# Performance work log

Hardware: AMD Instinct MI355X
Metric: run time of the kernel (lower is better)

Reference implementation:

```python
import jax, jax.numpy as jnp
import numpy as np

B, S, V, E, H = 1024, 256, 32000, 300, 256  # batch, enc_len, vocab, embed_dim, hidden_dim
ENC = 3 * H  # encoder feature width (768)


def setup_inputs() -> dict:
    key = jax.random.key(0)
    ks = jax.random.split(key, 14)
    s = 0.02
    return {
        "x": jax.random.randint(ks[0], (B,), 0, V),
        "h": jax.random.normal(ks[1], (B, H), jnp.float32),
        "c": jax.random.normal(ks[2], (B, H), jnp.float32),
        "encoder_outputs": jax.random.normal(ks[3], (B, S, ENC), jnp.float32),
        "emb": jax.random.normal(ks[4], (V, E), jnp.float32) * s,
        "attn_w": jax.random.normal(ks[5], (H, 4 * H), jnp.float32) * s,
        "attn_b": jnp.zeros((H,), jnp.float32),
        "v_w": jax.random.normal(ks[6], (H,), jnp.float32) * s,
        "w_ih": jax.random.normal(ks[7], (4 * H, E + ENC), jnp.float32) * s,
        "w_hh": jax.random.normal(ks[8], (4 * H, H), jnp.float32) * s,
        "b_ih": jnp.zeros((4 * H,), jnp.float32),
        "b_hh": jnp.zeros((4 * H,), jnp.float32),
        "out_w": jax.random.normal(ks[9], (V, H), jnp.float32) * s,
        "out_b": jnp.zeros((V,), jnp.float32),
    }


def reference(x, h, c, encoder_outputs, emb, attn_w, attn_b, v_w,
              w_ih, w_hh, b_ih, b_hh, out_w, out_b):
    # embedding (dropout is identity in eval mode)
    e = emb[x]  # [B, E]
    # additive attention: tanh(W [h; enc] + b); split W to avoid materializing the concat
    w_h, w_e = attn_w[:, :H], attn_w[:, H:]
    energy = jnp.tanh(h @ w_h.T[:, :] [None].squeeze(0) @ jnp.eye(H, dtype=h.dtype) if False else
                      (h @ w_h.T)[:, None, :] + jnp.einsum('bsd,hd->bsh', encoder_outputs, w_e) + attn_b)  # [B,S,H]
    scores = jnp.einsum('bsh,h->bs', energy, v_w)
    attn = jax.nn.softmax(scores, axis=1)  # [B,S]
    context = jnp.einsum('bs,bsd->bd', attn, encoder_outputs)  # [B, 3H]
    # single-step LSTM (PyTorch gate order: i, f, g, o)
    xi = jnp.concatenate([e, context], axis=-1)  # [B, E+3H]
    gates = xi @ w_ih.T + b_ih + h @ w_hh.T + b_hh  # [B, 4H]
    i, f, g, o = jnp.split(gates, 4, axis=-1)
    c2 = jax.nn.sigmoid(f) * c + jax.nn.sigmoid(i) * jnp.tanh(g)
    h2 = jax.nn.sigmoid(o) * jnp.tanh(c2)
    logits = h2 @ out_w.T + out_b  # [B, V]
    return logits, h2, c2
```

## Files before the change

### kernel.cpp

```cpp
#include <hip/hip_runtime.h>
#include <hip/hip_bf16.h>
#include <stdint.h>

#define BDIM 1024
#define SDIM 256
#define VDIM 32000
#define EDIM 300
#define HDIM 256
#define ENCD 768
#define G4H  1024
#define KXI  1344

typedef short bf16x8 __attribute__((ext_vector_type(8)));
typedef float f32x4  __attribute__((ext_vector_type(4)));

static __device__ __forceinline__ unsigned short f2bf(float f) {
  __hip_bfloat16 b = __float2bfloat16(f);
  return *reinterpret_cast<unsigned short*>(&b);
}
static __device__ __forceinline__ unsigned pk2(float x, float y) {
  float2 f; f.x = x; f.y = y;
  __hip_bfloat162 h = __float22bfloat162_rn(f);
  return *reinterpret_cast<unsigned*>(&h);
}
static __device__ __forceinline__ float bf2f(unsigned short u) {
  union { unsigned u; float f; } v; v.u = ((unsigned)u) << 16; return v.f;
}
static __device__ __forceinline__ float sigf(float x) {
  return 1.0f / (1.0f + __expf(-x));
}
static __device__ __forceinline__ float tanh_fast(float x) {
  return 1.0f - 2.0f / (__expf(2.0f * x) + 1.0f);
}
static __device__ __forceinline__ int swz_off(int row, int kbyte) {
  return row * 1536 + (kbyte ^ ((row & 7) << 4));
}

__global__ void k_prep(const float* __restrict__ attn_w, const float* __restrict__ w_ih,
                       const float* __restrict__ w_hh, const float* __restrict__ out_w,
                       const float* __restrict__ h,
                       unsigned short* __restrict__ w_e_frag, unsigned short* __restrict__ w_h_b,
                       unsigned short* __restrict__ h_b,
                       unsigned short* __restrict__ Wb, unsigned short* __restrict__ outw_b) {
  const long NWE = (long)HDIM * ENCD;
  const long NW1 = (long)HDIM * HDIM;
  const long NHB = (long)BDIM * HDIM;
  const long NWB = (long)G4H * KXI;
  const long NOW = (long)VDIM * HDIM;
  const long total = NWE + NW1 + NHB + NWB + NOW;
  for (long idx = blockIdx.x * 256L + threadIdx.x; idx < total; idx += gridDim.x * 256L) {
    long i = idx;
    if (i < NWE) {
      int e    = (int)(i & 7);
      int f    = (int)(i >> 3);
      int lane = f & 63;
      int n    = (f >> 6) & 1;
      int r2   = f >> 7;
      int kt   = r2 % 24;
      int w    = r2 / 24;
      int j    = 32 * w + 16 * n + (lane & 15);
      int k    = 32 * kt + (lane >> 4) * 8 + e;
      w_e_frag[i] = f2bf(attn_w[j * (4 * HDIM) + HDIM + k]);
    } else if ((i -= NWE) < NW1) {
      int j = (int)(i / HDIM), k = (int)(i % HDIM);
      w_h_b[i] = f2bf(attn_w[j * (4 * HDIM) + k]);
    } else if ((i -= NW1) < NHB) {
      h_b[i] = f2bf(h[i]);
    } else if ((i -= NHB) < NWB) {
      int g = (int)(i / KXI), k = (int)(i % KXI);
      float v = 0.f;
      if (k < EDIM + ENCD) v = w_ih[(long)g * (EDIM + ENCD) + k];
      else if (k < EDIM + ENCD + HDIM) v = w_hh[(long)g * HDIM + (k - (EDIM + ENCD))];
      Wb[i] = f2bf(v);
    } else {
      i -= NWB;
      outw_b[i] = f2bf(out_w[i]);
    }
  }
}

__launch_bounds__(512, 4)
__global__ void k_energy_ctx(const float* __restrict__ enc, const unsigned short* __restrict__ w_e_frag,
                             const float* __restrict__ hwb, const float* __restrict__ v_w,
                             float* __restrict__ ctx_part, float* __restrict__ denom_part) {
  const int b = blockIdx.x >> 3;
  const int st = blockIdx.x & 7;
  const int s0 = st * 32;
  const int t = threadIdx.x;
  const int lane = t & 63;
  const int w = t >> 6;
  const int li = lane & 15;
  const int lg = lane >> 4;

  __shared__ __align__(16) unsigned short encT[32 * ENCD];
  __shared__ float scores_lds[8 * 32];
  __shared__ float p_lds[32];

  const float* encB = enc + (long)(b * SDIM + s0) * ENCD;
  const int jw = 32 * w;
  const unsigned short* fragW = w_e_frag + (((long)w * 24 * 2) * 64 + lane) * 8;

  float4 sv[12];
#pragma unroll
  for (int u = 0; u < 12; ++u)
    sv[u] = *(const float4*)(encB + 4 * t + 2048 * u);

  bf16x8 bfr[6][2];
#pragma unroll
  for (int p = 0; p < 6; ++p)
#pragma unroll
    for (int n = 0; n < 2; ++n)
      bfr[p][n] = *(const bf16x8*)(fragW + ((p * 2 + n) * 64) * 8);

  float hw0 = hwb[b * HDIM + jw + li];
  float hw1 = hwb[b * HDIM + jw + 16 + li];
  float vw0 = v_w[jw + li];
  float vw1 = v_w[jw + 16 + li];

#pragma unroll
  for (int u = 0; u < 12; ++u) {
    const int flat = 4 * t + 2048 * u;
    const int row = flat / ENCD;
    const int col = flat - row * ENCD;
    uint2 pk;
    pk.x = pk2(sv[u].x, sv[u].y);
    pk.y = pk2(sv[u].z, sv[u].w);
    *(uint2*)((char*)encT + swz_off(row, col * 2)) = pk;
  }

  f32x4 acc[2][2];
#pragma unroll
  for (int m = 0; m < 2; m++)
#pragma unroll
    for (int n = 0; n < 2; n++) { f32x4 z = {0.f, 0.f, 0.f, 0.f}; acc[m][n] = z; }

  __syncthreads();

  bf16x8 afr[2][2];
#pragma unroll
  for (int p = 0; p < 2; ++p)
#pragma unroll
    for (int m = 0; m < 2; ++m)
      afr[p][m] = *(const bf16x8*)((const char*)encT + swz_off(16 * m + li, (p * 32 + lg * 8) * 2));

#pragma unroll
  for (int kt = 0; kt < 24; ++kt) {
    const int kb = kt % 6, ka = kt & 1;
#pragma unroll
    for (int m = 0; m < 2; m++)
#pragma unroll
      for (int n = 0; n < 2; n++)
        acc[m][n] = __builtin_amdgcn_mfma_f32_16x16x32_bf16(afr[ka][m], bfr[kb][n], acc[m][n], 0, 0, 0);
    if (kt + 6 < 24) {
#pragma unroll
      for (int n = 0; n < 2; ++n)
        bfr[kb][n] = *(const bf16x8*)(fragW + (((kt + 6) * 2 + n) * 64) * 8);
    }
    if (kt + 2 < 24) {
      const int kn2 = (kt + 2) * 32;
#pragma unroll
      for (int m = 0; m < 2; ++m)
        afr[ka][m] = *(const bf16x8*)((const char*)encT + swz_off(16 * m + li, (kn2 + lg * 8) * 2));
    }
  }

  float val[2][4];
#pragma unroll
  for (int m = 0; m < 2; m++)
#pragma unroll
    for (int r = 0; r < 4; r++) {
      float v0 = tanh_fast(acc[m][0][r] + hw0) * vw0 + tanh_fast(acc[m][1][r] + hw1) * vw1;
      v0 += __shfl_xor(v0, 1);
      v0 += __shfl_xor(v0, 2);
      v0 += __shfl_xor(v0, 4);
      v0 += __shfl_xor(v0, 8);
      val[m][r] = v0;
    }
  if (li < 4) {
    scores_lds[w * 32 + 4 * lg + li]      = val[0][li];
    scores_lds[w * 32 + 16 + 4 * lg + li] = val[1][li];
  }
  __syncthreads();
  if (t < 32) {
    float sc = 0.f;
#pragma unroll
    for (int ww = 0; ww < 8; ++ww) sc += scores_lds[ww * 32 + t];
    float p = __expf(sc);
    p_lds[t] = p;
    float dsum = p;
    dsum += __shfl_xor(dsum, 1);
    dsum += __shfl_xor(dsum, 2);
    dsum += __shfl_xor(dsum, 4);
    dsum += __shfl_xor(dsum, 8);
    dsum += __shfl_xor(dsum, 16);
    if (t == 0) denom_part[b * 8 + st] = dsum;
  }
  __syncthreads();
  if (t < 384) {
    float cx = 0.f, cy = 0.f;
#pragma unroll
    for (int s = 0; s < 32; ++s) {
      float p = p_lds[s];
      unsigned u = *(const unsigned*)((const char*)encT + swz_off(s, 4 * t));
      cx += p * bf2f((unsigned short)(u & 0xffffu));
      cy += p * bf2f((unsigned short)(u >> 16));
    }
    float* cp = ctx_part + (long)(b * 8 + st) * ENCD + 2 * t;
    cp[0] = cx; cp[1] = cy;
  }
}

__global__ void k_xi(const int* __restrict__ x, const float* __restrict__ emb,
                     const float* __restrict__ h, const float* __restrict__ ctx_part,
                     const float* __restrict__ denom_part, unsigned short* __restrict__ xi_b) {
  int b = blockIdx.x, t = threadIdx.x;
  float denom = 0.f;
#pragma unroll
  for (int st = 0; st < 8; ++st) denom += denom_part[b * 8 + st];
  float inv = 1.0f / denom;
#pragma unroll
  for (int u = 0; u < 3; ++u) {
    int d = t + 256 * u;
    float s = 0.f;
#pragma unroll
    for (int st = 0; st < 8; ++st) s += ctx_part[(long)(b * 8 + st) * ENCD + d];
    xi_b[(long)b * KXI + EDIM + d] = f2bf(s * inv);
  }
  int xv = x[b];
  for (int cc = t; cc < EDIM; cc += 256)
    xi_b[(long)b * KXI + cc] = f2bf(emb[(long)xv * EDIM + cc]);
  xi_b[(long)b * KXI + EDIM + ENCD + t] = f2bf(h[b * HDIM + t]);
  if (t < KXI - (EDIM + ENCD + HDIM))
    xi_b[(long)b * KXI + (EDIM + ENCD + HDIM) + t] = 0;
}

__launch_bounds__(256)
__global__ void k_gemm_bt(const unsigned short* __restrict__ A, const unsigned short* __restrict__ Bt,
                          const float* __restrict__ bias1, const float* __restrict__ bias2,
                          float* __restrict__ out, int N, int K, int MTILES) {
  int bx = blockIdx.x;
  int mt = bx % MTILES, nt = bx / MTILES;
  int row0 = mt * 128, col0 = nt * 128;
  int t = threadIdx.x, lane = t & 63, w = t >> 6;
  int li = lane & 15, lg = lane >> 4;
  int wr = (w >> 1) * 64, wc = (w & 1) * 64;
  __shared__ __align__(16) unsigned short As[2][128 * 32];
  __shared__ __align__(16) unsigned short Bs[2][128 * 32];
  f32x4 acc[4][4];
#pragma unroll
  for (int m = 0; m < 4; m++)
#pragma unroll
    for (int n = 0; n < 4; n++) { f32x4 z = {0.f, 0.f, 0.f, 0.f}; acc[m][n] = z; }

  auto stage = [&](int buf, int k0) {
#pragma unroll
    for (int rep = 0; rep < 2; ++rep) {
      int slot = t + rep * 256;
      int r = slot >> 2, sg = slot & 3;
      uint4 va = *(const uint4*)(A + (long)(row0 + r) * K + k0 + sg * 8);
      uint4 vb = *(const uint4*)(Bt + (long)(col0 + r) * K + k0 + sg * 8);
      *(uint4*)&As[buf][r * 32 + sg * 8] = va;
      *(uint4*)&Bs[buf][r * 32 + sg * 8] = vb;
    }
  };

  stage(0, 0);
  __syncthreads();
  const int nk = K / 32;
  for (int kt = 0; kt < nk; ++kt) {
    if (kt + 1 < nk) stage((kt + 1) & 1, (kt + 1) * 32);
    int cb = kt & 1;
    bf16x8 a[4], bb[4];
#pragma unroll
    for (int m = 0; m < 4; m++) a[m] = *(const bf16x8*)&As[cb][(wr + 16 * m + li) * 32 + lg * 8];
#pragma unroll
    for (int n = 0; n < 4; n++) bb[n] = *(const bf16x8*)&Bs[cb][(wc + 16 * n + li) * 32 + lg * 8];
#pragma unroll
    for (int m = 0; m < 4; m++)
#pragma unroll
      for (int n = 0; n < 4; n++)
        acc[m][n] = __builtin_amdgcn_mfma_f32_16x16x32_bf16(a[m], bb[n], acc[m][n], 0, 0, 0);
    __syncthreads();
  }

#pragma unroll
  for (int n = 0; n < 4; n++) {
    int col = col0 + wc + 16 * n + li;
    float bs = bias1[col];
    if (bias2) bs += bias2[col];
#pragma unroll
    for (int m = 0; m < 4; m++) {
      int rb = row0 + wr + 16 * m + lg * 4;
#pragma unroll
      for (int r = 0; r < 4; r++)
        out[(long)(rb + r) * N + col] = acc[m][n][r] + bs;
    }
  }
}

__global__ void k_lstm(const float* __restrict__ gates, const float* __restrict__ c,
                       float* __restrict__ h2, float* __restrict__ c2,
                       unsigned short* __restrict__ h2b) {
  int b = blockIdx.x, j = threadIdx.x;
  const float* g = gates + (long)b * G4H;
  float ig = sigf(g[j]);
  float fg = sigf(g[HDIM + j]);
  float gg = tanh_fast(g[2 * HDIM + j]);
  float og = sigf(g[3 * HDIM + j]);
  float cv = c[b * HDIM + j];
  float c2v = fg * cv + ig * gg;
  float h2v = og * tanh_fast(c2v);
  c2[b * HDIM + j] = c2v;
  h2[b * HDIM + j] = h2v;
  h2b[b * HDIM + j] = f2bf(h2v);
}

extern "C" void kernel_launch(void* const* d_in, const int* in_sizes, int n_in,
                              void* d_out, int out_size, void* d_ws, size_t ws_size,
                              hipStream_t stream) {
  const int*   x      = (const int*)d_in[0];
  const float* h      = (const float*)d_in[1];
  const float* c      = (const float*)d_in[2];
  const float* enc    = (const float*)d_in[3];
  const float* emb    = (const float*)d_in[4];
  const float* attn_w = (const float*)d_in[5];
  const float* attn_b = (const float*)d_in[6];
  const float* v_w    = (const float*)d_in[7];
  const float* w_ih   = (const float*)d_in[8];
  const float* w_hh   = (const float*)d_in[9];
  const float* b_ih   = (const float*)d_in[10];
  const float* b_hh   = (const float*)d_in[11];
  const float* out_w  = (const float*)d_in[12];
  const float* out_b  = (const float*)d_in[13];
  float* out = (float*)d_out;

  char* ws = (char*)d_ws;
  float* hwb             = (float*)(ws + 0);
  unsigned short* w_e_fr = (unsigned short*)(ws + 1048576);
  unsigned short* w_h_b  = (unsigned short*)(ws + 1441792);
  unsigned short* h_b    = (unsigned short*)(ws + 1572864);
  float* ctx_part        = (float*)(ws + 2097152);
  float* denom_part      = (float*)(ws + 27262976);
  unsigned short* Wb     = (unsigned short*)(ws + 27295744);
  unsigned short* xi_b   = (unsigned short*)(ws + 30048256);
  float* gates           = (float*)(ws + 32800768);
  unsigned short* h2b    = (unsigned short*)(ws + 36995072);
  unsigned short* outw_b = (unsigned short*)(ws + 37519360);
  if (ws_size < 53903360u) return;

  k_prep<<<2048, 256, 0, stream>>>(attn_w, w_ih, w_hh, out_w, h, w_e_fr, w_h_b, h_b, Wb, outw_b);
  k_gemm_bt<<<16, 256, 0, stream>>>(h_b, w_h_b, attn_b, nullptr, hwb, HDIM, HDIM, 8);
  k_energy_ctx<<<8192, 512, 0, stream>>>(enc, w_e_fr, hwb, v_w, ctx_part, denom_part);
  k_xi<<<1024, 256, 0, stream>>>(x, emb, h, ctx_part, denom_part, xi_b);
  k_gemm_bt<<<64, 256, 0, stream>>>(xi_b, Wb, b_ih, b_hh, gates, G4H, KXI, 8);
  k_lstm<<<1024, 256, 0, stream>>>(gates, c, out + (long)BDIM * VDIM,
                                   out + (long)BDIM * VDIM + (long)BDIM * HDIM, h2b);
  k_gemm_bt<<<2000, 256, 0, stream>>>(h2b, outw_b, out_b, nullptr, out, VDIM, HDIM, 8);
}
```

Measured before the change: 382.2 us.

## Make attention kernel persistent with async global-to-LDS prefetch and fused context reduction

Replaces the 8192-block energy/context kernel with 256 persistent blocks, each handling 32 consecutive (batch, seq-tile) units. The next encoder tile is prefetched straight into LDS with global_load_lds, so the load overlaps the current tile's MFMA work. Context and softmax denominator are accumulated in LDS across the 8 seq tiles of each batch row and written to xi_b as normalized bf16. This removes the ctx_part/denom_part round trip and the k_xi kernel, whose embedding, h and padding copies move into k_prep. In exchange occupancy drops to one 512-thread block per CU, with a large LDS footprint, and the loop becomes serial within each block.

Result: slower. 426.4 us (+11.5%).

```diff
diff --git a/kernel.cpp b/kernel.cpp
--- a/kernel.cpp
+++ b/kernel.cpp
@@ -14,6 +14,9 @@
 typedef short bf16x8 __attribute__((ext_vector_type(8)));
 typedef float f32x4  __attribute__((ext_vector_type(4)));
 
+typedef __attribute__((address_space(3))) void       lds_void;
+typedef const __attribute__((address_space(1))) void gbl_void;
+
 static __device__ __forceinline__ unsigned short f2bf(float f) {
   __hip_bfloat16 b = __float2bfloat16(f);
   return *reinterpret_cast<unsigned short*>(&b);
@@ -35,19 +38,30 @@
 static __device__ __forceinline__ int swz_off(int row, int kbyte) {
   return row * 1536 + (kbyte ^ ((row & 7) << 4));
 }
+static __device__ __forceinline__ void lds_barrier() {
+  asm volatile("s_waitcnt lgkmcnt(0)" ::: "memory");
+  __builtin_amdgcn_sched_barrier(0);
+  __builtin_amdgcn_s_barrier();
+  __builtin_amdgcn_sched_barrier(0);
+}
 
 __global__ void k_prep(const float* __restrict__ attn_w, const float* __restrict__ w_ih,
                        const float* __restrict__ w_hh, const float* __restrict__ out_w,
-                       const float* __restrict__ h,
+                       const float* __restrict__ h, const int* __restrict__ x,
+                       const float* __restrict__ emb,
                        unsigned short* __restrict__ w_e_frag, unsigned short* __restrict__ w_h_b,
                        unsigned short* __restrict__ h_b,
-                       unsigned short* __restrict__ Wb, unsigned short* __restrict__ outw_b) {
+                       unsigned short* __restrict__ Wb, unsigned short* __restrict__ outw_b,
+                       unsigned short* __restrict__ xi_b) {
   const long NWE = (long)HDIM * ENCD;
   const long NW1 = (long)HDIM * HDIM;
   const long NHB = (long)BDIM * HDIM;
   const long NWB = (long)G4H * KXI;
   const long NOW = (long)VDIM * HDIM;
-  const long total = NWE + NW1 + NHB + NWB + NOW;
+  const long NEM = (long)BDIM * EDIM;
+  const long NH2 = (long)BDIM * HDIM;
+  const long NPD = (long)BDIM * (KXI - (EDIM + ENCD + HDIM));
+  const long total = NWE + NW1 + NHB + NWB + NOW + NEM + NH2 + NPD;
   for (long idx = blockIdx.x * 256L + threadIdx.x; idx < total; idx += gridDim.x * 256L) {
     long i = idx;
     if (i < NWE) {
@@ -72,166 +86,187 @@
       if (k < EDIM + ENCD) v = w_ih[(long)g * (EDIM + ENCD) + k];
       else if (k < EDIM + ENCD + HDIM) v = w_hh[(long)g * HDIM + (k - (EDIM + ENCD))];
       Wb[i] = f2bf(v);
+    } else if ((i -= NWB) < NOW) {
+      outw_b[i] = f2bf(out_w[i]);
+    } else if ((i -= NOW) < NEM) {
+      int b = (int)(i / EDIM), cc = (int)(i % EDIM);
+      xi_b[(long)b * KXI + cc] = f2bf(emb[(long)x[b] * EDIM + cc]);
+    } else if ((i -= NEM) < NH2) {
+      int b = (int)(i / HDIM), j = (int)(i % HDIM);
+      xi_b[(long)b * KXI + EDIM + ENCD + j] = f2bf(h[(long)b * HDIM + j]);
     } else {
-      i -= NWB;
-      outw_b[i] = f2bf(out_w[i]);
-    }
-  }
-}
-
-__launch_bounds__(512, 4)
+      i -= NH2;
+      const int PADW = KXI - (EDIM + ENCD + HDIM);
+      int b = (int)(i / PADW), p = (int)(i % PADW);
+      xi_b[(long)b * KXI + EDIM + ENCD + HDIM + p] = 0;
+    }
+  }
+}
+
+__launch_bounds__(512, 1)
 __global__ void k_energy_ctx(const float* __restrict__ enc, const unsigned short* __restrict__ w_e_frag,
                              const float* __restrict__ hwb, const float* __restrict__ v_w,
-                             float* __restrict__ ctx_part, float* __restrict__ denom_part) {
-  const int b = blockIdx.x >> 3;
-  const int st = blockIdx.x & 7;
-  const int s0 = st * 32;
+                             unsigned short* __restrict__ xi_b) {
   const int t = threadIdx.x;
   const int lane = t & 63;
   const int w = t >> 6;
   const int li = lane & 15;
   const int lg = lane >> 4;
-
+  const int jw = 32 * w;
+
+  __shared__ __align__(16) float stageF[32 * ENCD];
   __shared__ __align__(16) unsigned short encT[32 * ENCD];
   __shared__ float scores_lds[8 * 32];
   __shared__ float p_lds[32];
-
-  const float* encB = enc + (long)(b * SDIM + s0) * ENCD;
-  const int jw = 32 * w;
-  const unsigned short* fragW = w_e_frag + (((long)w * 24 * 2) * 64 + lane) * 8;
-
-  float4 sv[12];
-#pragma unroll
-  for (int u = 0; u < 12; ++u)
-    sv[u] = *(const float4*)(encB + 4 * t + 2048 * u);
-
-  bf16x8 bfr[6][2];
-#pragma unroll
-  for (int p = 0; p < 6; ++p)
-#pragma unroll
-    for (int n = 0; n < 2; ++n)
-      bfr[p][n] = *(const bf16x8*)(fragW + ((p * 2 + n) * 64) * 8);
-
-  float hw0 = hwb[b * HDIM + jw + li];
-  float hw1 = hwb[b * HDIM + jw + 16 + li];
-  float vw0 = v_w[jw + li];
-  float vw1 = v_w[jw + 16 + li];
-
-#pragma unroll
-  for (int u = 0; u < 12; ++u) {
-    const int flat = 4 * t + 2048 * u;
-    const int row = flat / ENCD;
-    const int col = flat - row * ENCD;
-    uint2 pk;
-    pk.x = pk2(sv[u].x, sv[u].y);
-    pk.y = pk2(sv[u].z, sv[u].w);
-    *(uint2*)((char*)encT + swz_off(row, col * 2)) = pk;
-  }
-
-  f32x4 acc[2][2];
-#pragma unroll
-  for (int m = 0; m < 2; m++)
-#pragma unroll
-    for (int n = 0; n < 2; n++) { f32x4 z = {0.f, 0.f, 0.f, 0.f}; acc[m][n] = z; }
-
-  __syncthreads();
-
-  bf16x8 afr[2][2];
-#pragma unroll
-  for (int p = 0; p < 2; ++p)
-#pragma unroll
-    for (int m = 0; m < 2; ++m)
-      afr[p][m] = *(const bf16x8*)((const char*)encT + swz_off(16 * m + li, (p * 32 + lg * 8) * 2));
-
-#pragma unroll
-  for (int kt = 0; kt < 24; ++kt) {
-    const int kb = kt % 6, ka = kt & 1;
+  __shared__ float ctxAcc[ENCD];
+  __shared__ float hwb_lds[4 * HDIM];
+  __shared__ float denAcc;
+
+  const int NT = 32;
+  const int tile0 = blockIdx.x * NT;
+  const int b0 = tile0 >> 3;
+
+  {
+    const float* src = enc + (long)tile0 * 32 * ENCD;
+#pragma unroll
+    for (int u = 0; u < 12; ++u) {
+      const float* s = src + (u * 512 + t) * 4;
+      char* d = (char*)stageF + (u * 512 + (w << 6)) * 16;
+      __builtin_amdgcn_global_load_lds((gbl_void*)s, (lds_void*)d, 16, 0, 0);
+    }
+  }
+  hwb_lds[t]       = hwb[b0 * HDIM + t];
+  hwb_lds[t + 512] = hwb[b0 * HDIM + t + 512];
+  const float vw0 = v_w[jw + li];
+  const float vw1 = v_w[jw + 16 + li];
+  const unsigned short* fragW = w_e_frag + ((long)w * 3072 + lane) * 8;
+
+  for (int it = 0; it < NT; ++it) {
+    const int tile = tile0 + it;
+    const int b = tile >> 3, st = tile & 7;
+    const bool more = (it + 1 < NT);
+
+    __syncthreads();
+
+    if (st == 0) {
+      if (t < 384) { ctxAcc[2 * t] = 0.f; ctxAcc[2 * t + 1] = 0.f; }
+      if (t == 0) denAcc = 0.f;
+    }
+
+#pragma unroll
+    for (int u = 0; u < 12; ++u) {
+      const int s = u * 512 + t;
+      float4 v = *(const float4*)&stageF[4 * s];
+      const int flat = 4 * s;
+      const int row = flat / ENCD;
+      const int col = flat - row * ENCD;
+      uint2 pk;
+      pk.x = pk2(v.x, v.y);
+      pk.y = pk2(v.z, v.w);
+      *(uint2*)((char*)encT + swz_off(row, col * 2)) = pk;
+    }
+    lds_barrier();
+
+    if (more) {
+      const float* src = enc + (long)(tile + 1) * 32 * ENCD;
+#pragma unroll
+      for (int u = 0; u < 12; ++u) {
+        const float* s = src + (u * 512 + t) * 4;
+        char* d = (char*)stageF + (u * 512 + (w << 6)) * 16;
+        __builtin_amdgcn_global_load_lds((gbl_void*)s, (lds_void*)d, 16, 0, 0);
+      }
+    }
+
+    const float hw0 = hwb_lds[(b - b0) * HDIM + jw + li];
+    const float hw1 = hwb_lds[(b - b0) * HDIM + jw + 16 + li];
+
+    f32x4 acc[2][2];
 #pragma unroll
     for (int m = 0; m < 2; m++)
 #pragma unroll
-      for (int n = 0; n < 2; n++)
-        acc[m][n] = __builtin_amdgcn_mfma_f32_16x16x32_bf16(afr[ka][m], bfr[kb][n], acc[m][n], 0, 0, 0);
-    if (kt + 6 < 24) {
+      for (int n = 0; n < 2; n++) { f32x4 z = {0.f, 0.f, 0.f, 0.f}; acc[m][n] = z; }
+
+    bf16x8 bfr[4][2];
+#pragma unroll
+    for (int p = 0; p < 4; ++p)
 #pragma unroll
       for (int n = 0; n < 2; ++n)
-        bfr[kb][n] = *(const bf16x8*)(fragW + (((kt + 6) * 2 + n) * 64) * 8);
-    }
-    if (kt + 2 < 24) {
-      const int kn2 = (kt + 2) * 32;
-#pragma unroll
-      for (int m = 0; m < 2; ++m)
-        afr[ka][m] = *(const bf16x8*)((const char*)encT + swz_off(16 * m + li, (kn2 + lg * 8) * 2));
-    }
-  }
-
-  float val[2][4];
-#pragma unroll
-  for (int m = 0; m < 2; m++)
-#pragma unroll
-    for (int r = 0; r < 4; r++) {
-      float v0 = tanh_fast(acc[m][0][r] + hw0) * vw0 + tanh_fast(acc[m][1][r] + hw1) * vw1;
-      v0 += __shfl_xor(v0, 1);
-      v0 += __shfl_xor(v0, 2);
-      v0 += __shfl_xor(v0, 4);
-      v0 += __shfl_xor(v0, 8);
-      val[m][r] = v0;
-    }
-  if (li < 4) {
-    scores_lds[w * 32 + 4 * lg + li]      = val[0][li];
-    scores_lds[w * 32 + 16 + 4 * lg + li] = val[1][li];
-  }
-  __syncthreads();
-  if (t < 32) {
-    float sc = 0.f;
-#pragma unroll
-    for (int ww = 0; ww < 8; ++ww) sc += scores_lds[ww * 32 + t];
-    float p = __expf(sc);
-    p_lds[t] = p;
-    float dsum = p;
-    dsum += __shfl_xor(dsum, 1);
-    dsum += __shfl_xor(dsum, 2);
-    dsum += __shfl_xor(dsum, 4);
-    dsum += __shfl_xor(dsum, 8);
-    dsum += __shfl_xor(dsum, 16);
-    if (t == 0) denom_part[b * 8 + st] = dsum;
-  }
-  __syncthreads();
-  if (t < 384) {
-    float cx = 0.f, cy = 0.f;
-#pragma unroll
-    for (int s = 0; s < 32; ++s) {
-      float p = p_lds[s];
-      unsigned u = *(const unsigned*)((const char*)encT + swz_off(s, 4 * t));
-      cx += p * bf2f((unsigned short)(u & 0xffffu));
-      cy += p * bf2f((unsigned short)(u >> 16));
-    }
-    float* cp = ctx_part + (long)(b * 8 + st) * ENCD + 2 * t;
-    cp[0] = cx; cp[1] = cy;
-  }
-}
-
-__global__ void k_xi(const int* __restrict__ x, const float* __restrict__ emb,
-                     const float* __restrict__ h, const float* __restrict__ ctx_part,
-                     const float* __restrict__ denom_part, unsigned short* __restrict__ xi_b) {
-  int b = blockIdx.x, t = threadIdx.x;
-  float denom = 0.f;
-#pragma unroll
-  for (int st = 0; st < 8; ++st) denom += denom_part[b * 8 + st];
-  float inv = 1.0f / denom;
-#pragma unroll
-  for (int u = 0; u < 3; ++u) {
-    int d = t + 256 * u;
-    float s = 0.f;
-#pragma unroll
-    for (int st = 0; st < 8; ++st) s += ctx_part[(long)(b * 8 + st) * ENCD + d];
-    xi_b[(long)b * KXI + EDIM + d] = f2bf(s * inv);
-  }
-  int xv = x[b];
-  for (int cc = t; cc < EDIM; cc += 256)
-    xi_b[(long)b * KXI + cc] = f2bf(emb[(long)xv * EDIM + cc]);
-  xi_b[(long)b * KXI + EDIM + ENCD + t] = f2bf(h[b * HDIM + t]);
-  if (t < KXI - (EDIM + ENCD + HDIM))
-    xi_b[(long)b * KXI + (EDIM + ENCD + HDIM) + t] = 0;
+        bfr[p][n] = *(const bf16x8*)(fragW + ((p * 2 + n) * 64) * 8);
+
+#pragma unroll
+    for (int kt = 0; kt < 24; ++kt) {
+      const int kb = kt & 3;
+      bf16x8 a[2];
+#pragma unroll
+      for (int m = 0; m < 2; m++)
+        a[m] = *(const bf16x8*)((const char*)encT + swz_off(16 * m + li, (kt * 32 + lg * 8) * 2));
+#pragma unroll
+      for (int m = 0; m < 2; m++)
+#pragma unroll
+        for (int n = 0; n < 2; n++)
+          acc[m][n] = __builtin_amdgcn_mfma_f32_16x16x32_bf16(a[m], bfr[kb][n], acc[m][n], 0, 0, 0);
+      if (kt + 4 < 24) {
+#pragma unroll
+        for (int n = 0; n < 2; ++n)
+          bfr[kb][n] = *(const bf16x8*)(fragW + (((kt + 4) * 2 + n) * 64) * 8);
+      }
+    }
+
+    float val[2][4];
+#pragma unroll
+    for (int m = 0; m < 2; m++)
+#pragma unroll
+      for (int r = 0; r < 4; r++) {
+        float v0 = tanh_fast(acc[m][0][r] + hw0) * vw0 + tanh_fast(acc[m][1][r] + hw1) * vw1;
+        v0 += __shfl_xor(v0, 1);
+        v0 += __shfl_xor(v0, 2);
+        v0 += __shfl_xor(v0, 4);
+        v0 += __shfl_xor(v0, 8);
+        val[m][r] = v0;
+      }
+    if (li < 4) {
+      scores_lds[w * 32 + 4 * lg + li]      = val[0][li];
+      scores_lds[w * 32 + 16 + 4 * lg + li] = val[1][li];
+    }
+    lds_barrier();
+
+    if (t < 32) {
+      float sc = 0.f;
+#pragma unroll
+      for (int ww = 0; ww < 8; ++ww) sc += scores_lds[ww * 32 + t];
+      float p = __expf(sc);
+      p_lds[t] = p;
+      float dsum = p;
+      dsum += __shfl_xor(dsum, 1);
+      dsum += __shfl_xor(dsum, 2);
+      dsum += __shfl_xor(dsum, 4);
+      dsum += __shfl_xor(dsum, 8);
+      dsum += __shfl_xor(dsum, 16);
+      if (t == 0) denAcc += dsum;
+    }
+    lds_barrier();
+
+    if (t < 384) {
+      float cx = 0.f, cy = 0.f;
+#pragma unroll
+      for (int s = 0; s < 32; ++s) {
+        float p = p_lds[s];
+        unsigned u = *(const unsigned*)((const char*)encT + swz_off(s, 4 * t));
+        cx += p * bf2f((unsigned short)(u & 0xffffu));
+        cy += p * bf2f((unsigned short)(u >> 16));
+      }
+      cx += ctxAcc[2 * t];
+      cy += ctxAcc[2 * t + 1];
+      if (st == 7) {
+        const float inv = 1.0f / denAcc;
+        unsigned pk = (unsigned)f2bf(cx * inv) | ((unsigned)f2bf(cy * inv) << 16);
+        *(unsigned*)&xi_b[(long)b * KXI + EDIM + 2 * t] = pk;
+      } else {
+        ctxAcc[2 * t]     = cx;
+        ctxAcc[2 * t + 1] = cy;
+      }
+    }
+  }
 }
 
 __launch_bounds__(256)
@@ -339,19 +374,17 @@
   unsigned short* w_e_fr = (unsigned short*)(ws + 1048576);
   unsigned short* w_h_b  = (unsigned short*)(ws + 1441792);
   unsigned short* h_b    = (unsigned short*)(ws + 1572864);
-  float* ctx_part        = (float*)(ws + 2097152);
-  float* denom_part      = (float*)(ws + 27262976);
-  unsigned short* Wb     = (unsigned short*)(ws + 27295744);
-  unsigned short* xi_b   = (unsigned short*)(ws + 30048256);
-  float* gates           = (float*)(ws + 32800768);
-  unsigned short* h2b    = (unsigned short*)(ws + 36995072);
-  unsigned short* outw_b = (unsigned short*)(ws + 37519360);
-  if (ws_size < 53903360u) return;
-
-  k_prep<<<2048, 256, 0, stream>>>(attn_w, w_ih, w_hh, out_w, h, w_e_fr, w_h_b, h_b, Wb, outw_b);
+  unsigned short* Wb     = (unsigned short*)(ws + 2097152);
+  unsigned short* xi_b   = (unsigned short*)(ws + 4849664);
+  float* gates           = (float*)(ws + 7602176);
+  unsigned short* h2b    = (unsigned short*)(ws + 11796480);
+  unsigned short* outw_b = (unsigned short*)(ws + 12320768);
+  if (ws_size < 28704768u) return;
+
+  k_prep<<<2048, 256, 0, stream>>>(attn_w, w_ih, w_hh, out_w, h, x, emb,
+                                   w_e_fr, w_h_b, h_b, Wb, outw_b, xi_b);
   k_gemm_bt<<<16, 256, 0, stream>>>(h_b, w_h_b, attn_b, nullptr, hwb, HDIM, HDIM, 8);
-  k_energy_ctx<<<8192, 512, 0, stream>>>(enc, w_e_fr, hwb, v_w, ctx_part, denom_part);
-  k_xi<<<1024, 256, 0, stream>>>(x, emb, h, ctx_part, denom_part, xi_b);
+  k_energy_ctx<<<256, 512, 0, stream>>>(enc, w_e_fr, hwb, v_w, xi_b);
   k_gemm_bt<<<64, 256, 0, stream>>>(xi_b, Wb, b_ih, b_hh, gates, G4H, KXI, 8);
   k_lstm<<<1024, 256, 0, stream>>>(gates, c, out + (long)BDIM * VDIM,
                                    out + (long)BDIM * VDIM + (long)BDIM * HDIM, h2b);
```

## Double sequence tile per block in energy kernel so waves share W_e fragments

Applied to the files above, without the earlier changes.

Each energy/context block now handles 64 sequence positions with 1024 threads (16 waves), where two groups of 8 waves split the rows and reuse the same per-wave W_e column slice. That halves the number of partial context/denominator records, which shrinks the workspace and the reduction in k_xi. The A-fragment prefetch is replaced by direct per-step LDS loads and the B prefetch depth drops from 6 to 4. The cost is 96KB of LDS and launch bounds of 1024,1, which limit each CU to one resident block and cut latency hiding.

Result: slower. 444.6 us (+16.3%).

```diff
diff --git a/kernel.cpp b/kernel.cpp
--- a/kernel.cpp
+++ b/kernel.cpp
@@ -79,35 +79,37 @@
   }
 }
 
-__launch_bounds__(512, 4)
+__launch_bounds__(1024, 1)
 __global__ void k_energy_ctx(const float* __restrict__ enc, const unsigned short* __restrict__ w_e_frag,
                              const float* __restrict__ hwb, const float* __restrict__ v_w,
                              float* __restrict__ ctx_part, float* __restrict__ denom_part) {
-  const int b = blockIdx.x >> 3;
-  const int st = blockIdx.x & 7;
-  const int s0 = st * 32;
+  const int b = blockIdx.x >> 2;
+  const int st = blockIdx.x & 3;
+  const int s0 = st * 64;
   const int t = threadIdx.x;
   const int lane = t & 63;
   const int w = t >> 6;
   const int li = lane & 15;
   const int lg = lane >> 4;
-
-  __shared__ __align__(16) unsigned short encT[32 * ENCD];
-  __shared__ float scores_lds[8 * 32];
-  __shared__ float p_lds[32];
+  const int sh = w >> 3;
+  const int jq = w & 7;
+  const int jw = 32 * jq;
+
+  __shared__ __align__(16) unsigned short encT[64 * ENCD];
+  __shared__ float scores_lds[16 * 32];
+  __shared__ float p_lds[64];
 
   const float* encB = enc + (long)(b * SDIM + s0) * ENCD;
-  const int jw = 32 * w;
-  const unsigned short* fragW = w_e_frag + (((long)w * 24 * 2) * 64 + lane) * 8;
+  const unsigned short* fragW = w_e_frag + ((long)jq * 3072 + lane) * 8;
 
   float4 sv[12];
 #pragma unroll
   for (int u = 0; u < 12; ++u)
-    sv[u] = *(const float4*)(encB + 4 * t + 2048 * u);
-
-  bf16x8 bfr[6][2];
-#pragma unroll
-  for (int p = 0; p < 6; ++p)
+    sv[u] = *(const float4*)(encB + 4 * t + 4096 * u);
+
+  bf16x8 bfr[4][2];
+#pragma unroll
+  for (int p = 0; p < 4; ++p)
 #pragma unroll
     for (int n = 0; n < 2; ++n)
       bfr[p][n] = *(const bf16x8*)(fragW + ((p * 2 + n) * 64) * 8);
@@ -119,7 +121,7 @@
 
 #pragma unroll
   for (int u = 0; u < 12; ++u) {
-    const int flat = 4 * t + 2048 * u;
+    const int flat = 4 * t + 4096 * u;
     const int row = flat / ENCD;
     const int col = flat - row * ENCD;
     uint2 pk;
@@ -136,31 +138,24 @@
 
   __syncthreads();
 
-  bf16x8 afr[2][2];
-#pragma unroll
-  for (int p = 0; p < 2; ++p)
-#pragma unroll
-    for (int m = 0; m < 2; ++m)
-      afr[p][m] = *(const bf16x8*)((const char*)encT + swz_off(16 * m + li, (p * 32 + lg * 8) * 2));
-
 #pragma unroll
   for (int kt = 0; kt < 24; ++kt) {
-    const int kb = kt % 6, ka = kt & 1;
+    const int kb = kt & 3;
+    bf16x8 a[2];
+#pragma unroll
+    for (int m = 0; m < 2; m++) {
+      const int row = sh * 32 + 16 * m + li;
+      a[m] = *(const bf16x8*)((const char*)encT + swz_off(row, (kt * 32 + lg * 8) * 2));
+    }
 #pragma unroll
     for (int m = 0; m < 2; m++)
 #pragma unroll
       for (int n = 0; n < 2; n++)
-        acc[m][n] = __builtin_amdgcn_mfma_f32_16x16x32_bf16(afr[ka][m], bfr[kb][n], acc[m][n], 0, 0, 0);
-    if (kt + 6 < 24) {
+        acc[m][n] = __builtin_amdgcn_mfma_f32_16x16x32_bf16(a[m], bfr[kb][n], acc[m][n], 0, 0, 0);
+    if (kt + 4 < 24) {
 #pragma unroll
       for (int n = 0; n < 2; ++n)
-        bfr[kb][n] = *(const bf16x8*)(fragW + (((kt + 6) * 2 + n) * 64) * 8);
-    }
-    if (kt + 2 < 24) {
-      const int kn2 = (kt + 2) * 32;
-#pragma unroll
-      for (int m = 0; m < 2; ++m)
-        afr[ka][m] = *(const bf16x8*)((const char*)encT + swz_off(16 * m + li, (kn2 + lg * 8) * 2));
+        bfr[kb][n] = *(const bf16x8*)(fragW + (((kt + 4) * 2 + n) * 64) * 8);
     }
   }
 
@@ -181,10 +176,11 @@
     scores_lds[w * 32 + 16 + 4 * lg + li] = val[1][li];
   }
   __syncthreads();
-  if (t < 32) {
+  if (t < 64) {
+    const int half = t >> 5, r = t & 31;
     float sc = 0.f;
 #pragma unroll
-    for (int ww = 0; ww < 8; ++ww) sc += scores_lds[ww * 32 + t];
+    for (int k = 0; k < 8; ++k) sc += scores_lds[(half * 8 + k) * 32 + r];
     float p = __expf(sc);
     p_lds[t] = p;
     float dsum = p;
@@ -193,19 +189,20 @@
     dsum += __shfl_xor(dsum, 4);
     dsum += __shfl_xor(dsum, 8);
     dsum += __shfl_xor(dsum, 16);
-    if (t == 0) denom_part[b * 8 + st] = dsum;
+    dsum += __shfl_xor(dsum, 32);
+    if (t == 0) denom_part[b * 4 + st] = dsum;
   }
   __syncthreads();
   if (t < 384) {
     float cx = 0.f, cy = 0.f;
-#pragma unroll
-    for (int s = 0; s < 32; ++s) {
+#pragma unroll 8
+    for (int s = 0; s < 64; ++s) {
       float p = p_lds[s];
       unsigned u = *(const unsigned*)((const char*)encT + swz_off(s, 4 * t));
       cx += p * bf2f((unsigned short)(u & 0xffffu));
       cy += p * bf2f((unsigned short)(u >> 16));
     }
-    float* cp = ctx_part + (long)(b * 8 + st) * ENCD + 2 * t;
+    float* cp = ctx_part + (long)(b * 4 + st) * ENCD + 2 * t;
     cp[0] = cx; cp[1] = cy;
   }
 }
@@ -216,14 +213,14 @@
   int b = blockIdx.x, t = threadIdx.x;
   float denom = 0.f;
 #pragma unroll
-  for (int st = 0; st < 8; ++st) denom += denom_part[b * 8 + st];
+  for (int st = 0; st < 4; ++st) denom += denom_part[b * 4 + st];
   float inv = 1.0f / denom;
 #pragma unroll
   for (int u = 0; u < 3; ++u) {
     int d = t + 256 * u;
     float s = 0.f;
 #pragma unroll
-    for (int st = 0; st < 8; ++st) s += ctx_part[(long)(b * 8 + st) * ENCD + d];
+    for (int st = 0; st < 4; ++st) s += ctx_part[(long)(b * 4 + st) * ENCD + d];
     xi_b[(long)b * KXI + EDIM + d] = f2bf(s * inv);
   }
   int xv = x[b];
@@ -340,17 +337,17 @@
   unsigned short* w_h_b  = (unsigned short*)(ws + 1441792);
   unsigned short* h_b    = (unsigned short*)(ws + 1572864);
   float* ctx_part        = (float*)(ws + 2097152);
-  float* denom_part      = (float*)(ws + 27262976);
-  unsigned short* Wb     = (unsigned short*)(ws + 27295744);
-  unsigned short* xi_b   = (unsigned short*)(ws + 30048256);
-  float* gates           = (float*)(ws + 32800768);
-  unsigned short* h2b    = (unsigned short*)(ws + 36995072);
-  unsigned short* outw_b = (unsigned short*)(ws + 37519360);
-  if (ws_size < 53903360u) return;
+  float* denom_part      = (float*)(ws + 14680064);
+  unsigned short* Wb     = (unsigned short*)(ws + 14696448);
+  unsigned short* xi_b   = (unsigned short*)(ws + 17448960);
+  float* gates           = (float*)(ws + 20201472);
+  unsigned short* h2b    = (unsigned short*)(ws + 24395776);
+  unsigned short* outw_b = (unsigned short*)(ws + 24920064);
+  if (ws_size < 41304064u) return;
 
   k_prep<<<2048, 256, 0, stream>>>(attn_w, w_ih, w_hh, out_w, h, w_e_fr, w_h_b, h_b, Wb, outw_b);
   k_gemm_bt<<<16, 256, 0, stream>>>(h_b, w_h_b, attn_b, nullptr, hwb, HDIM, HDIM, 8);
-  k_energy_ctx<<<8192, 512, 0, stream>>>(enc, w_e_fr, hwb, v_w, ctx_part, denom_part);
+  k_energy_ctx<<<4096, 1024, 0, stream>>>(enc, w_e_fr, hwb, v_w, ctx_part, denom_part);
   k_xi<<<1024, 256, 0, stream>>>(x, emb, h, ctx_part, denom_part, xi_b);
   k_gemm_bt<<<64, 256, 0, stream>>>(xi_b, Wb, b_ih, b_hh, gates, G4H, KXI, 8);
   k_lstm<<<1024, 256, 0, stream>>>(gates, c, out + (long)BDIM * VDIM,
```
